# Optimization experiments

Measured on AMD Instinct MI355X. Metric: run time of the kernel, lower is better.

## Reference

```python
import jax, jax.numpy as jnp
import numpy as np

UNITS = 1024
NUM_HEADS = 16
MASK_VALUE = -1e12


def setup_inputs() -> dict:
    key = jax.random.key(0)
    k1, k2, k3, k4 = jax.random.split(key, 4)
    B, S = 8, 1024
    memory = jax.random.normal(k1, (B, S, 2 * UNITS), dtype=jnp.float32)
    query = jax.random.normal(k2, (B, S, UNITS), dtype=jnp.float32)
    b = jax.random.normal(k3, (S,), dtype=jnp.float32)
    seq_len = jax.random.randint(k4, (B, 1), 0, S, dtype=jnp.int32)
    return {"memory": memory, "query": query, "b": b, "seq_len": seq_len}


def _split_heads(x, n):
    # [B, S, D] -> [B, n, S, D/n]
    B, S, D = x.shape
    return x.reshape(B, S, n, D // n).transpose(0, 2, 1, 3)


def reference(memory, query, b, seq_len):
    B, S, _ = query.shape
    dh = UNITS // NUM_HEADS
    k_mem, v_mem = jnp.split(memory, 2, axis=2)
    Q = _split_heads(query, NUM_HEADS) * (dh ** -0.5)   # [B,H,S,dh]
    Kh = _split_heads(k_mem, NUM_HEADS)                  # [B,H,S,dh]
    Vh = _split_heads(v_mem, NUM_HEADS)                  # [B,H,S,dh]
    logits = jnp.einsum('bhqd,bhkd->bhqk', Q, Kh) + b    # bias broadcast over keys
    # mask: one_hot(seq_len) -> cumsum -> 1-cumsum == (pos < seq_len)
    valid = (jnp.arange(S)[None, :] < seq_len[:, 0:1]).astype(jnp.float32)  # [B,S]
    logits = logits + MASK_VALUE * (1.0 - valid)[:, None, None, :]
    weights = jax.nn.softmax(logits, axis=-1)
    out = jnp.einsum('bhqk,bhkd->bhqd', weights, Vh)
    return out.transpose(0, 2, 1, 3).reshape(B, S, UNITS)
```

## Files before the change

### kernel.cpp

```cpp
#include <hip/hip_runtime.h>

#define B_      8
#define S_      1024
#define H_      16
#define DH      64
#define UNITS_  1024
#define MSTRIDE 2048
#define KVB     64
#define QTB     128
#define LP      72
#define LOG2E   1.4426950408889634f

typedef __attribute__((ext_vector_type(8))) short bf16x8;
typedef __attribute__((ext_vector_type(4))) short bf16x4;
typedef __attribute__((ext_vector_type(4))) float f32x4;

__device__ __forceinline__ unsigned cvt_pk_bf16(float lo, float hi) {
    unsigned r;
    asm("v_cvt_pk_bf16_f32 %0, %1, %2" : "=v"(r) : "v"(lo), "v"(hi));
    return r;
}

__global__ __launch_bounds__(256, 4)
void attn_kernel(const float* __restrict__ mem, const float* __restrict__ qry,
                 const float* __restrict__ bias, const int* __restrict__ slen,
                 float* __restrict__ out)
{
    __shared__ alignas(16) unsigned short Ks[KVB][LP];
    __shared__ alignas(16) unsigned short Vs[KVB * DH];
    __shared__ alignas(16) unsigned short Ps[4][16][LP];

    const int tid  = threadIdx.x;
    const int wq   = tid >> 6;
    const int lane = tid & 63;
    const int lr   = lane & 15;
    const int lg   = lane >> 4;

    const int qt = blockIdx.x;
    const int h  = blockIdx.y;
    const int b  = blockIdx.z;

    int L = slen[b];
    if (L == 0) L = S_;
    const int ntiles = (L + KVB - 1) / KVB;

    const float* qp = qry + ((size_t)(b * S_ + qt * QTB)) * UNITS_ + h * DH;
    const float* kp = mem + ((size_t)b * S_) * MSTRIDE + h * DH;
    const float* vp = kp + UNITS_;
    float*       op = out + ((size_t)(b * S_ + qt * QTB)) * UNITS_ + h * DH;

    bf16x8 qf[2][2];
    #pragma unroll
    for (int rb = 0; rb < 2; ++rb)
      #pragma unroll
      for (int kc = 0; kc < 2; ++kc) {
        const float* qrow = qp + (size_t)(wq*32 + rb*16 + lr) * UNITS_ + kc*32 + lg*8;
        float4 f0 = ((const float4*)qrow)[0];
        float4 f1 = ((const float4*)qrow)[1];
        const float sc = 0.125f * LOG2E;
        uint4 u;
        u.x = cvt_pk_bf16(f0.x*sc, f0.y*sc);
        u.y = cvt_pk_bf16(f0.z*sc, f0.w*sc);
        u.z = cvt_pk_bf16(f1.x*sc, f1.y*sc);
        u.w = cvt_pk_bf16(f1.z*sc, f1.w*sc);
        qf[rb][kc] = __builtin_bit_cast(bf16x8, u);
      }

    f32x4 o[2][4];
    float ls[2][4];
    #pragma unroll
    for (int rb = 0; rb < 2; ++rb)
      #pragma unroll
      for (int r = 0; r < 4; ++r) {
        o[rb][r] = (f32x4){0.f,0.f,0.f,0.f};
        ls[rb][r] = 0.f;
      }

    const unsigned vsb = (unsigned)(uintptr_t)&Vs[0];
    const int krow = tid >> 2;
    const int dblk = tid & 3;

    for (int t = 0; t < ntiles; ++t) {
        const int kvb = t * KVB;
        {
            const float4* ks = (const float4*)(kp + (size_t)(kvb + krow) * MSTRIDE + dblk * 16);
            float4 a0 = ks[0], a1 = ks[1], a2 = ks[2], a3 = ks[3];
            uint4 w0, w1;
            w0.x = cvt_pk_bf16(a0.x, a0.y); w0.y = cvt_pk_bf16(a0.z, a0.w);
            w0.z = cvt_pk_bf16(a1.x, a1.y); w0.w = cvt_pk_bf16(a1.z, a1.w);
            w1.x = cvt_pk_bf16(a2.x, a2.y); w1.y = cvt_pk_bf16(a2.z, a2.w);
            w1.z = cvt_pk_bf16(a3.x, a3.y); w1.w = cvt_pk_bf16(a3.z, a3.w);
            uint4* d = (uint4*)&Ks[krow][dblk * 16];
            d[0] = w0; d[1] = w1;
        }
        {
            const float* vr = vp + (size_t)(kvb + krow) * MSTRIDE;
            #pragma unroll
            for (int i = 0; i < 4; ++i) {
                const int rot = (i + (krow >> 2)) & 3;
                const int d0  = dblk * 16 + rot * 4;
                float4 f = *(const float4*)(vr + d0);
                uint2 w;
                w.x = cvt_pk_bf16(f.x, f.y);
                w.y = cvt_pk_bf16(f.z, f.w);
                const int e = ((krow >> 2) << 8) + ((d0 >> 4) << 6) + ((krow & 3) << 4) + (d0 & 15);
                *(uint2*)&Vs[e] = w;
            }
        }
        __syncthreads();

        float bv[4];
        #pragma unroll
        for (int cb = 0; cb < 4; ++cb) {
            const int key = kvb + cb * 16 + lr;
            bv[cb] = (key < L) ? bias[key] * LOG2E : -INFINITY;
        }

        bf16x4 vt[2][4][2];
        #pragma unroll
        for (int kc = 0; kc < 2; ++kc)
          #pragma unroll
          for (int c = 0; c < 4; ++c) {
            unsigned a1 = vsb + ((kc * 8 + lg * 2) << 9) + (c << 7) + (lr << 3);
            asm volatile("ds_read_b64_tr_b16 %0, %1" : "=v"(vt[kc][c][0]) : "v"(a1));
            asm volatile("ds_read_b64_tr_b16 %0, %1 offset:512" : "=v"(vt[kc][c][1]) : "v"(a1));
          }

        #pragma unroll
        for (int rb = 0; rb < 2; ++rb) {
            f32x4 s[4];
            #pragma unroll
            for (int cb = 0; cb < 4; ++cb) {
                f32x4 acc = (f32x4){0.f,0.f,0.f,0.f};
                #pragma unroll
                for (int kc = 0; kc < 2; ++kc) {
                    bf16x8 kf = *(const bf16x8*)&Ks[cb * 16 + lr][kc * 32 + lg * 8];
                    acc = __builtin_amdgcn_mfma_f32_16x16x32_bf16(qf[rb][kc], kf, acc, 0, 0, 0);
                }
                s[cb] = acc;
            }
            #pragma unroll
            for (int cb = 0; cb < 4; ++cb)
                #pragma unroll
                for (int r = 0; r < 4; ++r) {
                    float e = exp2f(s[cb][r] + bv[cb]);
                    s[cb][r] = e;
                    ls[rb][r] += e;
                }
            asm volatile("" ::: "memory");
            #pragma unroll
            for (int cb = 0; cb < 4; ++cb)
                #pragma unroll
                for (int r = 0; r < 4; r += 2) {
                    unsigned u = cvt_pk_bf16(s[cb][r], s[cb][r + 1]);
                    Ps[wq][lg * 4 + r][((cb ^ lg) & 3) * 16 + lr]     = (unsigned short)u;
                    Ps[wq][lg * 4 + r + 1][((cb ^ lg) & 3) * 16 + lr] = (unsigned short)(u >> 16);
                }
            asm volatile("s_waitcnt lgkmcnt(0)" ::: "memory");
            __builtin_amdgcn_sched_barrier(0);
            #pragma unroll
            for (int kc = 0; kc < 2; ++kc) {
                bf16x8 pf = *(const bf16x8*)&Ps[wq][lr][((((kc * 2) + (lg >> 1)) ^ ((lr >> 2) & 3)) << 4) + ((lg & 1) << 3)];
                #pragma unroll
                for (int c = 0; c < 4; ++c) {
                    bf16x8 vf = __builtin_shufflevector(vt[kc][c][0], vt[kc][c][1], 0,1,2,3,4,5,6,7);
                    o[rb][c] = __builtin_amdgcn_mfma_f32_16x16x32_bf16(pf, vf, o[rb][c], 0, 0, 0);
                }
            }
        }
        __syncthreads();
    }

    #pragma unroll
    for (int rb = 0; rb < 2; ++rb)
        #pragma unroll
        for (int r = 0; r < 4; ++r) {
            float v = ls[rb][r];
            v += __shfl_xor(v, 1, 64);
            v += __shfl_xor(v, 2, 64);
            v += __shfl_xor(v, 4, 64);
            v += __shfl_xor(v, 8, 64);
            const float inv = 1.0f / v;
            float* orow = op + (size_t)(wq * 32 + rb * 16 + lg * 4 + r) * UNITS_;
            #pragma unroll
            for (int c = 0; c < 4; ++c)
                orow[c * 16 + lr] = o[rb][c][r] * inv;
        }
}

extern "C" void kernel_launch(void* const* d_in, const int* in_sizes, int n_in,
                              void* d_out, int out_size, void* d_ws, size_t ws_size,
                              hipStream_t stream) {
    const float* mem  = (const float*)d_in[0];
    const float* qry  = (const float*)d_in[1];
    const float* bias = (const float*)d_in[2];
    const int*   slen = (const int*)d_in[3];
    float*       out  = (float*)d_out;
    dim3 grid(S_ / QTB, H_, B_);
    attn_kernel<<<grid, dim3(256), 0, stream>>>(mem, qry, bias, slen, out);
}
```

Before: 230.3 us.

## Halve query tile, prefetch next KV tile into registers, transpose P via LDS

Halves the query tile per block from 128 to 64 rows (one 16-row block per wave), which doubles the grid and the number of times K/V is loaded. Prefetches the next K/V tile from global memory into registers while the current tile is computed. Also replaces K padding with an XOR swizzle and stores P transposed so it can be read with ds_read_b64_tr_b16. The aim is to hide global-load latency and add parallelism, at the cost of doubled K/V global traffic and conversion work.

```diff
diff --git a/kernel.cpp b/kernel.cpp
--- a/kernel.cpp
+++ b/kernel.cpp
@@ -1,14 +1,12 @@
 #include <hip/hip_runtime.h>
 
-#define B_      8
 #define S_      1024
 #define H_      16
 #define DH      64
 #define UNITS_  1024
 #define MSTRIDE 2048
 #define KVB     64
-#define QTB     128
-#define LP      72
+#define QTB     64
 #define LOG2E   1.4426950408889634f
 
 typedef __attribute__((ext_vector_type(8))) short bf16x8;
@@ -26,9 +24,9 @@
                  const float* __restrict__ bias, const int* __restrict__ slen,
                  float* __restrict__ out)
 {
-    __shared__ alignas(16) unsigned short Ks[KVB][LP];
+    __shared__ alignas(16) unsigned short Ks[KVB][DH];
     __shared__ alignas(16) unsigned short Vs[KVB * DH];
-    __shared__ alignas(16) unsigned short Ps[4][16][LP];
+    __shared__ alignas(16) unsigned short Pt[4][KVB][16];
 
     const int tid  = threadIdx.x;
     const int wq   = tid >> 6;
@@ -49,12 +47,10 @@
     const float* vp = kp + UNITS_;
     float*       op = out + ((size_t)(b * S_ + qt * QTB)) * UNITS_ + h * DH;
 
-    bf16x8 qf[2][2];
+    bf16x8 qf[2];
     #pragma unroll
-    for (int rb = 0; rb < 2; ++rb)
-      #pragma unroll
-      for (int kc = 0; kc < 2; ++kc) {
-        const float* qrow = qp + (size_t)(wq*32 + rb*16 + lr) * UNITS_ + kc*32 + lg*8;
+    for (int kc = 0; kc < 2; ++kc) {
+        const float* qrow = qp + (size_t)(wq*16 + lr) * UNITS_ + kc*32 + lg*8;
         float4 f0 = ((const float4*)qrow)[0];
         float4 f1 = ((const float4*)qrow)[1];
         const float sc = 0.125f * LOG2E;
@@ -63,129 +59,142 @@
         u.y = cvt_pk_bf16(f0.z*sc, f0.w*sc);
         u.z = cvt_pk_bf16(f1.x*sc, f1.y*sc);
         u.w = cvt_pk_bf16(f1.z*sc, f1.w*sc);
-        qf[rb][kc] = __builtin_bit_cast(bf16x8, u);
-      }
-
-    f32x4 o[2][4];
-    float ls[2][4];
+        qf[kc] = __builtin_bit_cast(bf16x8, u);
+    }
+
+    f32x4 o[4];
+    float ls4[4];
     #pragma unroll
-    for (int rb = 0; rb < 2; ++rb)
-      #pragma unroll
-      for (int r = 0; r < 4; ++r) {
-        o[rb][r] = (f32x4){0.f,0.f,0.f,0.f};
-        ls[rb][r] = 0.f;
-      }
-
-    const unsigned vsb = (unsigned)(uintptr_t)&Vs[0];
+    for (int r = 0; r < 4; ++r) { o[r] = (f32x4){0.f,0.f,0.f,0.f}; ls4[r] = 0.f; }
+
     const int krow = tid >> 2;
     const int dblk = tid & 3;
+    const int rotb = (krow >> 2) & 3;
+    const unsigned ksw0 = (unsigned)((dblk*16)     ^ ((krow & 7) * 8));
+    const unsigned ksw1 = (unsigned)((dblk*16 + 8) ^ ((krow & 7) * 8));
+    const int vbase = ((krow >> 2) << 8) | (dblk << 6) | ((krow & 3) << 4);
+    const int r0 = (0 + rotb) & 3, r1 = (1 + rotb) & 3, r2 = (2 + rotb) & 3, r3 = (3 + rotb) & 3;
+
+    const float* krow_p = kp + (size_t)krow * MSTRIDE + dblk * 16;
+    const float* vrow_p = vp + (size_t)krow * MSTRIDE + dblk * 16;
+
+    float4 pk0, pk1, pk2, pk3, pv0, pv1, pv2, pv3;
+    {
+        const float4* ksrc = (const float4*)krow_p;
+        pk0 = ksrc[0]; pk1 = ksrc[1]; pk2 = ksrc[2]; pk3 = ksrc[3];
+        pv0 = *(const float4*)(vrow_p + r0*4);
+        pv1 = *(const float4*)(vrow_p + r1*4);
+        pv2 = *(const float4*)(vrow_p + r2*4);
+        pv3 = *(const float4*)(vrow_p + r3*4);
+    }
+
+    const unsigned ptw = (unsigned)(uintptr_t)&Pt[wq][0][0];
+    const unsigned vsb = (unsigned)(uintptr_t)&Vs[0];
 
     for (int t = 0; t < ntiles; ++t) {
         const int kvb = t * KVB;
         {
-            const float4* ks = (const float4*)(kp + (size_t)(kvb + krow) * MSTRIDE + dblk * 16);
-            float4 a0 = ks[0], a1 = ks[1], a2 = ks[2], a3 = ks[3];
             uint4 w0, w1;
-            w0.x = cvt_pk_bf16(a0.x, a0.y); w0.y = cvt_pk_bf16(a0.z, a0.w);
-            w0.z = cvt_pk_bf16(a1.x, a1.y); w0.w = cvt_pk_bf16(a1.z, a1.w);
-            w1.x = cvt_pk_bf16(a2.x, a2.y); w1.y = cvt_pk_bf16(a2.z, a2.w);
-            w1.z = cvt_pk_bf16(a3.x, a3.y); w1.w = cvt_pk_bf16(a3.z, a3.w);
-            uint4* d = (uint4*)&Ks[krow][dblk * 16];
-            d[0] = w0; d[1] = w1;
-        }
-        {
-            const float* vr = vp + (size_t)(kvb + krow) * MSTRIDE;
+            w0.x = cvt_pk_bf16(pk0.x, pk0.y); w0.y = cvt_pk_bf16(pk0.z, pk0.w);
+            w0.z = cvt_pk_bf16(pk1.x, pk1.y); w0.w = cvt_pk_bf16(pk1.z, pk1.w);
+            w1.x = cvt_pk_bf16(pk2.x, pk2.y); w1.y = cvt_pk_bf16(pk2.z, pk2.w);
+            w1.z = cvt_pk_bf16(pk3.x, pk3.y); w1.w = cvt_pk_bf16(pk3.z, pk3.w);
+            *(uint4*)&Ks[krow][ksw0] = w0;
+            *(uint4*)&Ks[krow][ksw1] = w1;
+            uint2 v0, v1, v2, v3;
+            v0.x = cvt_pk_bf16(pv0.x, pv0.y); v0.y = cvt_pk_bf16(pv0.z, pv0.w);
+            v1.x = cvt_pk_bf16(pv1.x, pv1.y); v1.y = cvt_pk_bf16(pv1.z, pv1.w);
+            v2.x = cvt_pk_bf16(pv2.x, pv2.y); v2.y = cvt_pk_bf16(pv2.z, pv2.w);
+            v3.x = cvt_pk_bf16(pv3.x, pv3.y); v3.y = cvt_pk_bf16(pv3.z, pv3.w);
+            *(uint2*)&Vs[vbase + r0*4] = v0;
+            *(uint2*)&Vs[vbase + r1*4] = v1;
+            *(uint2*)&Vs[vbase + r2*4] = v2;
+            *(uint2*)&Vs[vbase + r3*4] = v3;
+        }
+        __syncthreads();
+
+        if (t + 1 < ntiles) {
+            const float* kn = krow_p + (size_t)(t + 1) * KVB * MSTRIDE;
+            const float* vn = vrow_p + (size_t)(t + 1) * KVB * MSTRIDE;
+            const float4* ksrc = (const float4*)kn;
+            pk0 = ksrc[0]; pk1 = ksrc[1]; pk2 = ksrc[2]; pk3 = ksrc[3];
+            pv0 = *(const float4*)(vn + r0*4);
+            pv1 = *(const float4*)(vn + r1*4);
+            pv2 = *(const float4*)(vn + r2*4);
+            pv3 = *(const float4*)(vn + r3*4);
+        }
+
+        float bv[4];
+        #pragma unroll
+        for (int cb = 0; cb < 4; ++cb) {
+            const int key = kvb + cb*16 + lr;
+            bv[cb] = (key < L) ? bias[key] * LOG2E : -INFINITY;
+        }
+
+        f32x4 s[4];
+        #pragma unroll
+        for (int cb = 0; cb < 4; ++cb) {
+            f32x4 acc = (f32x4){0.f,0.f,0.f,0.f};
             #pragma unroll
-            for (int i = 0; i < 4; ++i) {
-                const int rot = (i + (krow >> 2)) & 3;
-                const int d0  = dblk * 16 + rot * 4;
-                float4 f = *(const float4*)(vr + d0);
-                uint2 w;
-                w.x = cvt_pk_bf16(f.x, f.y);
-                w.y = cvt_pk_bf16(f.z, f.w);
-                const int e = ((krow >> 2) << 8) + ((d0 >> 4) << 6) + ((krow & 3) << 4) + (d0 & 15);
-                *(uint2*)&Vs[e] = w;
+            for (int kc = 0; kc < 2; ++kc) {
+                bf16x8 kf = *(const bf16x8*)&Ks[cb*16 + lr][(unsigned)(kc*32 + lg*8) ^ ((unsigned)(lr & 7) * 8)];
+                acc = __builtin_amdgcn_mfma_f32_16x16x32_bf16(qf[kc], kf, acc, 0, 0, 0);
             }
-        }
-        __syncthreads();
-
-        float bv[4];
+            s[cb] = acc;
+        }
+
         #pragma unroll
         for (int cb = 0; cb < 4; ++cb) {
-            const int key = kvb + cb * 16 + lr;
-            bv[cb] = (key < L) ? bias[key] * LOG2E : -INFINITY;
-        }
-
-        bf16x4 vt[2][4][2];
-        #pragma unroll
-        for (int kc = 0; kc < 2; ++kc)
-          #pragma unroll
-          for (int c = 0; c < 4; ++c) {
-            unsigned a1 = vsb + ((kc * 8 + lg * 2) << 9) + (c << 7) + (lr << 3);
-            asm volatile("ds_read_b64_tr_b16 %0, %1" : "=v"(vt[kc][c][0]) : "v"(a1));
-            asm volatile("ds_read_b64_tr_b16 %0, %1 offset:512" : "=v"(vt[kc][c][1]) : "v"(a1));
-          }
-
-        #pragma unroll
-        for (int rb = 0; rb < 2; ++rb) {
-            f32x4 s[4];
+            float e0 = exp2f(s[cb][0] + bv[cb]);
+            float e1 = exp2f(s[cb][1] + bv[cb]);
+            float e2 = exp2f(s[cb][2] + bv[cb]);
+            float e3 = exp2f(s[cb][3] + bv[cb]);
+            ls4[0] += e0; ls4[1] += e1; ls4[2] += e2; ls4[3] += e3;
+            uint2 u;
+            u.x = cvt_pk_bf16(e0, e1);
+            u.y = cvt_pk_bf16(e2, e3);
+            *(uint2*)&Pt[wq][cb*16 + lr][lg*4] = u;
+        }
+        asm volatile("" ::: "memory");
+
+        #pragma unroll
+        for (int kc = 0; kc < 2; ++kc) {
+            bf16x4 p0, p1;
+            unsigned pa = ptw + (unsigned)((kc*8 + lg*2) << 7) + (unsigned)(lr << 3);
+            asm volatile("ds_read_b64_tr_b16 %0, %1" : "=v"(p0) : "v"(pa));
+            asm volatile("ds_read_b64_tr_b16 %0, %1 offset:128" : "=v"(p1) : "v"(pa));
+            bf16x4 vt0[4], vt1[4];
             #pragma unroll
-            for (int cb = 0; cb < 4; ++cb) {
-                f32x4 acc = (f32x4){0.f,0.f,0.f,0.f};
-                #pragma unroll
-                for (int kc = 0; kc < 2; ++kc) {
-                    bf16x8 kf = *(const bf16x8*)&Ks[cb * 16 + lr][kc * 32 + lg * 8];
-                    acc = __builtin_amdgcn_mfma_f32_16x16x32_bf16(qf[rb][kc], kf, acc, 0, 0, 0);
-                }
-                s[cb] = acc;
+            for (int c = 0; c < 4; ++c) {
+                unsigned va = vsb + (unsigned)((kc*8 + lg*2) << 9) + (unsigned)(c << 7) + (unsigned)(lr << 3);
+                asm volatile("ds_read_b64_tr_b16 %0, %1" : "=v"(vt0[c]) : "v"(va));
+                asm volatile("ds_read_b64_tr_b16 %0, %1 offset:512" : "=v"(vt1[c]) : "v"(va));
             }
-            #pragma unroll
-            for (int cb = 0; cb < 4; ++cb)
-                #pragma unroll
-                for (int r = 0; r < 4; ++r) {
-                    float e = exp2f(s[cb][r] + bv[cb]);
-                    s[cb][r] = e;
-                    ls[rb][r] += e;
-                }
-            asm volatile("" ::: "memory");
-            #pragma unroll
-            for (int cb = 0; cb < 4; ++cb)
-                #pragma unroll
-                for (int r = 0; r < 4; r += 2) {
-                    unsigned u = cvt_pk_bf16(s[cb][r], s[cb][r + 1]);
-                    Ps[wq][lg * 4 + r][((cb ^ lg) & 3) * 16 + lr]     = (unsigned short)u;
-                    Ps[wq][lg * 4 + r + 1][((cb ^ lg) & 3) * 16 + lr] = (unsigned short)(u >> 16);
-                }
             asm volatile("s_waitcnt lgkmcnt(0)" ::: "memory");
             __builtin_amdgcn_sched_barrier(0);
+            bf16x8 pf = __builtin_shufflevector(p0, p1, 0,1,2,3,4,5,6,7);
             #pragma unroll
-            for (int kc = 0; kc < 2; ++kc) {
-                bf16x8 pf = *(const bf16x8*)&Ps[wq][lr][((((kc * 2) + (lg >> 1)) ^ ((lr >> 2) & 3)) << 4) + ((lg & 1) << 3)];
-                #pragma unroll
-                for (int c = 0; c < 4; ++c) {
-                    bf16x8 vf = __builtin_shufflevector(vt[kc][c][0], vt[kc][c][1], 0,1,2,3,4,5,6,7);
-                    o[rb][c] = __builtin_amdgcn_mfma_f32_16x16x32_bf16(pf, vf, o[rb][c], 0, 0, 0);
-                }
+            for (int c = 0; c < 4; ++c) {
+                bf16x8 vf = __builtin_shufflevector(vt0[c], vt1[c], 0,1,2,3,4,5,6,7);
+                o[c] = __builtin_amdgcn_mfma_f32_16x16x32_bf16(pf, vf, o[c], 0, 0, 0);
             }
         }
         __syncthreads();
     }
 
     #pragma unroll
-    for (int rb = 0; rb < 2; ++rb)
-        #pragma unroll
-        for (int r = 0; r < 4; ++r) {
-            float v = ls[rb][r];
-            v += __shfl_xor(v, 1, 64);
-            v += __shfl_xor(v, 2, 64);
-            v += __shfl_xor(v, 4, 64);
-            v += __shfl_xor(v, 8, 64);
-            const float inv = 1.0f / v;
-            float* orow = op + (size_t)(wq * 32 + rb * 16 + lg * 4 + r) * UNITS_;
-            #pragma unroll
-            for (int c = 0; c < 4; ++c)
-                orow[c * 16 + lr] = o[rb][c][r] * inv;
-        }
+    for (int r = 0; r < 4; ++r) {
+        float v = ls4[r];
+        v += __shfl_xor(v, 1, 64);
+        v += __shfl_xor(v, 2, 64);
+        v += __shfl_xor(v, 4, 64);
+        v += __shfl_xor(v, 8, 64);
+        const float inv = 1.0f / v;
+        float* orow = op + (size_t)(wq*16 + lg*4 + r) * UNITS_;
+        #pragma unroll
+        for (int c = 0; c < 4; ++c)
+            orow[c*16 + lr] = o[c][r] * inv;
+    }
 }
 
 extern "C" void kernel_launch(void* const* d_in, const int* in_sizes, int n_in,
@@ -196,6 +205,6 @@
     const float* bias = (const float*)d_in[2];
     const int*   slen = (const int*)d_in[3];
     float*       out  = (float*)d_out;
-    dim3 grid(S_ / QTB, H_, B_);
+    dim3 grid(S_ / QTB, H_, 8);
     attn_kernel<<<grid, dim3(256), 0, stream>>>(mem, qry, bias, slen, out);
 }
```

Measured after the change: 196.5 us. -14.7%, faster.
